# Kernel tuning notes

Hardware: AMD Instinct MI355X
Metric: run time of the kernel (lower is better)

Reference implementation:

```python
import jax, jax.numpy as jnp
import numpy as np

WS = 8            # window size (square)
N = WS * WS       # tokens per window = 64
DIM = 192
HEADS = 6
HDIM = DIM // HEADS
SCALE = HDIM ** -0.5


def _rel_pos_index(ws=WS):
    coords = np.stack(np.meshgrid(np.arange(ws), np.arange(ws), indexing='ij'))  # [2,ws,ws]
    cf = coords.reshape(2, -1)                       # [2, N]
    rc = (cf[:, :, None] - cf[:, None, :]).transpose(1, 2, 0).astype(np.int64)  # [N,N,2]
    rc[:, :, 0] += ws - 1
    rc[:, :, 1] += ws - 1
    rc[:, :, 0] *= 2 * ws - 1
    return jnp.asarray(rc.sum(-1))                   # [N, N]

REL_IDX = _rel_pos_index()


def _linear(x, w, b=None):
    y = jnp.einsum('...i,oi->...o', x, w)
    return y if b is None else y + b


def _diff_attn(q_t, k_t, v_t, q_r, k_r, v_r, bias, lam):
    # q,k,v: [B, H, N, d]; bias: [H, N, N]; lam scalar
    at = jax.nn.softmax(jnp.einsum('bhqd,bhkd->bhqk', q_t * SCALE, k_t) + bias, axis=-1)
    ar = jax.nn.softmax(jnp.einsum('bhqd,bhkd->bhqk', q_r * SCALE, k_r) + bias, axis=-1)
    dt = at - lam * ar
    dr = ar - lam * at
    ot = jnp.einsum('bhqk,bhkd->bhqd', dt, v_t)
    orf = jnp.einsum('bhqk,bhkd->bhqd', dr, v_r)
    return ot, orf


def _heads(x, B):
    # [B, N, C] -> [B, H, N, d]
    return x.reshape(B, N, HEADS, HDIM).transpose(0, 2, 1, 3)


def _unheads(x, B):
    return x.transpose(0, 2, 1, 3).reshape(B, N, DIM)


def setup_inputs() -> dict:
    key = jax.random.key(0)
    ks = jax.random.split(key, 16)
    nW = 1024
    p = lambda k, shp: (jax.random.normal(k, shp, jnp.float32) * 0.02)
    return {
        'x_windows': jax.random.normal(ks[0], (nW, N, DIM), jnp.float32),
        'y_windows': jax.random.normal(ks[1], (nW, N, DIM), jnp.float32),
        'sa_qkv_w': p(ks[2], (3 * DIM, DIM)), 'sa_qkv_b': jnp.zeros((3 * DIM,), jnp.float32),
        'sa_ct_w': p(ks[3], (DIM, DIM)), 'sa_cr_w': p(ks[4], (DIM, DIM)),
        'ca_q_w': p(ks[5], (DIM, DIM)), 'ca_q_b': jnp.zeros((DIM,), jnp.float32),
        'ca_kv_w': p(ks[6], (2 * DIM, DIM)), 'ca_kv_b': jnp.zeros((2 * DIM,), jnp.float32),
        'ca_ct_w': p(ks[7], (DIM, DIM)), 'ca_cr_w': p(ks[8], (DIM, DIM)),
        'rpb_table': p(ks[9], ((2 * WS - 1) * (2 * WS - 1), HEADS)),
        'proj_sa_w': p(ks[10], (DIM, DIM)), 'proj_sa_b': jnp.zeros((DIM,), jnp.float32),
        'proj_ca_w': p(ks[11], (DIM, DIM)), 'proj_ca_b': jnp.zeros((DIM,), jnp.float32),
        'lambda_sa': jnp.float32(0.1), 'lambda_ca': jnp.float32(0.1),
        'sa_enh': jnp.float32(0.1), 'ca_enh': jnp.float32(0.1),
    }


def reference(x_windows, y_windows, sa_qkv_w, sa_qkv_b, sa_ct_w, sa_cr_w,
              ca_q_w, ca_q_b, ca_kv_w, ca_kv_b, ca_ct_w, ca_cr_w,
              rpb_table, proj_sa_w, proj_sa_b, proj_ca_w, proj_ca_b,
              lambda_sa, lambda_ca, sa_enh, ca_enh):
    B = x_windows.shape[0]
    bias = rpb_table[REL_IDX.reshape(-1)].reshape(N, N, HEADS).transpose(2, 0, 1)  # [H,N,N]

    # ---- Self-attention branch (batch-dim concat) ----
    t_enh = x_windows + sa_enh * _linear(y_windows, sa_cr_w)
    r_enh = y_windows + sa_enh * _linear(x_windows, sa_ct_w)
    qkv_t = _linear(t_enh, sa_qkv_w, sa_qkv_b).reshape(B, N, 3, HEADS, HDIM).transpose(2, 0, 3, 1, 4)
    qkv_r = _linear(r_enh, sa_qkv_w, sa_qkv_b).reshape(B, N, 3, HEADS, HDIM).transpose(2, 0, 3, 1, 4)
    lam_sa = jnp.clip(jax.nn.sigmoid(lambda_sa), 0.01, 0.99)
    ot, orf = _diff_attn(qkv_t[0], qkv_t[1], qkv_t[2], qkv_r[0], qkv_r[1], qkv_r[2], bias, lam_sa)
    sa_t = _linear(_unheads(ot, B), proj_sa_w, proj_sa_b)
    sa_r = _linear(_unheads(orf, B), proj_sa_w, proj_sa_b)
    sa_out = jnp.concatenate([sa_t, sa_r], axis=0)  # [2B, N, C]

    # ---- Cross-attention branch (seq-dim concat) ----
    t_enh = x_windows + ca_enh * _linear(y_windows, ca_cr_w)
    r_enh = y_windows + ca_enh * _linear(x_windows, ca_ct_w)
    q_t = _heads(_linear(t_enh, ca_q_w, ca_q_b), B)
    q_r = _heads(_linear(r_enh, ca_q_w, ca_q_b), B)
    xcat = jnp.concatenate([t_enh, r_enh], axis=1)  # [B, 2N, C]
    kv = _linear(xcat, ca_kv_w, ca_kv_b).reshape(B, 2 * N, 2, HEADS, HDIM).transpose(2, 0, 3, 1, 4)
    k, v = kv[0], kv[1]
    k_t, k_r = k[:, :, :N], k[:, :, N:]
    v_t, v_r = v[:, :, :N], v[:, :, N:]
    lam_ca = jnp.clip(jax.nn.sigmoid(lambda_ca), 0.01, 0.99)
    ot, orf = _diff_attn(q_t, k_t, v_t, q_r, k_r, v_r, bias, lam_ca)
    ca_t = _linear(_unheads(ot, B), proj_ca_w, proj_ca_b)
    ca_r = _linear(_unheads(orf, B), proj_ca_w, proj_ca_b)
    ca_out = jnp.concatenate([ca_t, ca_r], axis=1)  # [B, 2N, C]

    # pack into a single array: [4B, N, C]
    return jnp.concatenate([sa_out, ca_out.reshape(2 * B, N, DIM)], axis=0)
```

## Files before the change

### kernel.cpp

```cpp
#include <hip/hip_runtime.h>

#define KD 192
#define H6 6

typedef __attribute__((ext_vector_type(8))) short bf16x8;
typedef __attribute__((ext_vector_type(4))) float f32x4;

__device__ __forceinline__ unsigned short f2bf(float f) {
  unsigned u = __float_as_uint(f);
  u += 0x7FFFu + ((u >> 16) & 1u);
  return (unsigned short)(u >> 16);
}

__global__ void bias_k(const float* __restrict__ tab, float* __restrict__ biasw) {
  int t = blockIdx.x * 256 + threadIdx.x;
  if (t >= H6 * 64 * 64) return;
  int h = t >> 12, rem = t & 4095, i = rem >> 6, j = rem & 63;
  int idx = ((i >> 3) - (j >> 3) + 7) * 15 + ((i & 7) - (j & 7) + 7);
  biasw[t] = tab[idx * H6 + h];
}

__global__ void convert_k(
    const float* __restrict__ sa_qkv_w, const float* __restrict__ sa_ct_w,
    const float* __restrict__ sa_cr_w, const float* __restrict__ ca_q_w,
    const float* __restrict__ ca_kv_w, const float* __restrict__ ca_ct_w,
    const float* __restrict__ ca_cr_w, const float* __restrict__ proj_sa_w,
    const float* __restrict__ proj_ca_w,
    const float* __restrict__ ca_q_b, const float* __restrict__ ca_kv_b,
    unsigned short* __restrict__ wqkv, unsigned short* __restrict__ wct_sa,
    unsigned short* __restrict__ wcr_sa, unsigned short* __restrict__ wca,
    unsigned short* __restrict__ wct_ca, unsigned short* __restrict__ wcr_ca,
    unsigned short* __restrict__ wpsa, unsigned short* __restrict__ wpca,
    float* __restrict__ bca)
{
  int t = blockIdx.x * 256 + threadIdx.x;
  if (t < 110592) {
    int i = t << 2;
    const float* s; unsigned short* d;
    if (i < 110592)      { s = sa_qkv_w + i;            d = wqkv + i; }
    else if (i < 147456) { s = sa_ct_w + (i - 110592);  d = wct_sa + (i - 110592); }
    else if (i < 184320) { s = sa_cr_w + (i - 147456);  d = wcr_sa + (i - 147456); }
    else if (i < 221184) { s = ca_q_w + (i - 184320);   d = wca + (i - 184320); }
    else if (i < 294912) { s = ca_kv_w + (i - 221184);  d = wca + 36864 + (i - 221184); }
    else if (i < 331776) { s = ca_ct_w + (i - 294912);  d = wct_ca + (i - 294912); }
    else if (i < 368640) { s = ca_cr_w + (i - 331776);  d = wcr_ca + (i - 331776); }
    else if (i < 405504) { s = proj_sa_w + (i - 368640); d = wpsa + (i - 368640); }
    else                 { s = proj_ca_w + (i - 405504); d = wpca + (i - 405504); }
    float4 v = *(const float4*)s;
    ushort4 p;
    p.x = f2bf(v.x); p.y = f2bf(v.y); p.z = f2bf(v.z); p.w = f2bf(v.w);
    *(ushort4*)d = p;
  } else if (t < 110592 + 144) {
    int i = (t - 110592) << 2;
    const float* s = (i < 192) ? (ca_q_b + i) : (ca_kv_b + (i - 192));
    *(float4*)(bca + i) = *(const float4*)s;
  }
}

__global__ __launch_bounds__(256) void enh_k(
    const float* __restrict__ x, const float* __restrict__ y,
    const unsigned short* __restrict__ wcr_sa, const unsigned short* __restrict__ wct_sa,
    const unsigned short* __restrict__ wcr_ca, const unsigned short* __restrict__ wct_ca,
    const float* __restrict__ sap, const float* __restrict__ cap,
    unsigned short* __restrict__ e0, unsigned short* __restrict__ e1,
    unsigned short* __restrict__ e2, unsigned short* __restrict__ e3)
{
  __shared__ short Xl[64][200], Yl[64][200], Wl[64][200];
  const int tid = threadIdx.x;
  const int nblk = blockIdx.x, mblk = blockIdx.y;
  const int row = tid >> 2, cb = (tid & 3) * 48;
  {
    const float* xp = x + ((long)mblk * 64 + row) * KD + cb;
    const float* yp = y + ((long)mblk * 64 + row) * KD + cb;
#pragma unroll
    for (int j = 0; j < 12; ++j) {
      float4 vx = *(const float4*)(xp + 4 * j);
      float4 vy = *(const float4*)(yp + 4 * j);
      ushort4 px, py;
      px.x = f2bf(vx.x); px.y = f2bf(vx.y); px.z = f2bf(vx.z); px.w = f2bf(vx.w);
      py.x = f2bf(vy.x); py.y = f2bf(vy.y); py.z = f2bf(vy.z); py.w = f2bf(vy.w);
      *(ushort4*)&Xl[row][cb + 4 * j] = px;
      *(ushort4*)&Yl[row][cb + 4 * j] = py;
    }
  }
  const unsigned short* Ws[4] = {wcr_sa, wct_sa, wcr_ca, wct_ca};
  unsigned short* Es[4] = {e0, e1, e2, e3};
  const float s_sa = *sap, s_ca = *cap;

  const int lane = tid & 63, wv = tid >> 6;
  const int qn = lane & 15, g = lane >> 4;
  const int mloc = 16 * wv + 4 * g;
  const f32x4 zero = {0.f, 0.f, 0.f, 0.f};

  for (int it = 0; it < 4; ++it) {
    {
      const unsigned short* Wp = Ws[it] + ((long)nblk * 64 + row) * KD + cb;
#pragma unroll
      for (int j = 0; j < 6; ++j)
        *(float4*)&Wl[row][cb + 8 * j] = *(const float4*)(Wp + 8 * j);
    }
    __syncthreads();
    short (*Aloc)[200] = (it & 1) ? Xl : Yl;
    f32x4 acc[4];
#pragma unroll
    for (int nt = 0; nt < 4; ++nt) acc[nt] = zero;
#pragma unroll
    for (int ks = 0; ks < 6; ++ks) {
      bf16x8 a = *(const bf16x8*)&Aloc[16 * wv + qn][32 * ks + 8 * g];
#pragma unroll
      for (int nt = 0; nt < 4; ++nt) {
        bf16x8 bfr = *(const bf16x8*)&Wl[16 * nt + qn][32 * ks + 8 * g];
        acc[nt] = __builtin_amdgcn_mfma_f32_16x16x32_bf16(a, bfr, acc[nt], 0, 0, 0);
      }
    }
    const float* resid = (it & 1) ? y : x;
    const float sc = (it < 2) ? s_sa : s_ca;
    unsigned short* dst = Es[it];
#pragma unroll
    for (int nt = 0; nt < 4; ++nt) {
      const int c = nblk * 64 + 16 * nt + qn;
#pragma unroll
      for (int r = 0; r < 4; ++r) {
        const long m = (long)mblk * 64 + mloc + r;
        dst[m * KD + c] = f2bf(resid[m * KD + c] + sc * acc[nt][r]);
      }
    }
    __syncthreads();
  }
}

struct QkvArgs {
  const unsigned short* A[4];
  const unsigned short* W[4];
  const float* bias[4];
  unsigned short* dq[4];
  unsigned short* dk[4];
  unsigned short* dv[4];
};

__global__ __launch_bounds__(256) void qkv_k(QkvArgs args, float SC)
{
  __shared__ short Al[64][200], Wl[64][200];
  const int tid = threadIdx.x;
  const int nblk = blockIdx.x, mblk = blockIdx.y, z = blockIdx.z;
  const int row = tid >> 2, cb = (tid & 3) * 48;
  {
    const unsigned short* A = args.A[z] + ((long)mblk * 64 + row) * KD + cb;
#pragma unroll
    for (int j = 0; j < 6; ++j)
      *(float4*)&Al[row][cb + 8 * j] = *(const float4*)(A + 8 * j);
    const unsigned short* Wp = args.W[z] + ((long)nblk * 64 + row) * KD + cb;
#pragma unroll
    for (int j = 0; j < 6; ++j)
      *(float4*)&Wl[row][cb + 8 * j] = *(const float4*)(Wp + 8 * j);
  }
  __syncthreads();

  const int lane = tid & 63, wv = tid >> 6;
  const int qn = lane & 15, g = lane >> 4;
  const f32x4 zero = {0.f, 0.f, 0.f, 0.f};
  f32x4 acc[4];
#pragma unroll
  for (int nt = 0; nt < 4; ++nt) acc[nt] = zero;
#pragma unroll
  for (int ks = 0; ks < 6; ++ks) {
    bf16x8 a = *(const bf16x8*)&Al[16 * wv + qn][32 * ks + 8 * g];
#pragma unroll
    for (int nt = 0; nt < 4; ++nt) {
      bf16x8 bfr = *(const bf16x8*)&Wl[16 * nt + qn][32 * ks + 8 * g];
      acc[nt] = __builtin_amdgcn_mfma_f32_16x16x32_bf16(a, bfr, acc[nt], 0, 0, 0);
    }
  }
  const int mloc = 16 * wv + 4 * g;
#pragma unroll
  for (int nt = 0; nt < 4; ++nt) {
    const int cg = nblk * 64 + 16 * nt + qn;
    const int idx = (cg >= 384) ? 2 : ((cg >= 192) ? 1 : 0);
    const int cc = cg - idx * KD;
    const int h = cc >> 5, d = cc & 31;
    const float bv = args.bias[z][cg];
    const float sca = (idx == 0) ? SC : 1.f;
    const long bwh = (long)mblk * H6 + h;
    if (idx < 2) {
      unsigned short* dst = idx ? args.dk[z] : args.dq[z];
#pragma unroll
      for (int r = 0; r < 4; ++r)
        dst[(bwh * 64 + (mloc + r)) * 32 + d] = f2bf((acc[nt][r] + bv) * sca);
    } else {
      ushort4 p;
      p.x = f2bf(acc[nt][0] + bv);
      p.y = f2bf(acc[nt][1] + bv);
      p.z = f2bf(acc[nt][2] + bv);
      p.w = f2bf(acc[nt][3] + bv);
      *(ushort4*)&args.dv[z][(bwh * 32 + d) * 64 + mloc] = p;
    }
  }
}

struct ProjArgs {
  const unsigned short* A[4];
  const unsigned short* W[4];
  const float* bias[4];
  float* o[4];
  long wstride[4];
};

__global__ __launch_bounds__(256) void proj_k(ProjArgs args)
{
  __shared__ short Al[64][200], Wl[64][200];
  const int tid = threadIdx.x;
  const int nblk = blockIdx.x, mblk = blockIdx.y, z = blockIdx.z;
  const int row = tid >> 2, cb = (tid & 3) * 48;
  {
    const unsigned short* A = args.A[z] + ((long)mblk * 64 + row) * KD + cb;
#pragma unroll
    for (int j = 0; j < 6; ++j)
      *(float4*)&Al[row][cb + 8 * j] = *(const float4*)(A + 8 * j);
    const unsigned short* Wp = args.W[z] + ((long)nblk * 64 + row) * KD + cb;
#pragma unroll
    for (int j = 0; j < 6; ++j)
      *(float4*)&Wl[row][cb + 8 * j] = *(const float4*)(Wp + 8 * j);
  }
  __syncthreads();

  const int lane = tid & 63, wv = tid >> 6;
  const int qn = lane & 15, g = lane >> 4;
  const f32x4 zero = {0.f, 0.f, 0.f, 0.f};
  f32x4 acc[4];
#pragma unroll
  for (int nt = 0; nt < 4; ++nt) acc[nt] = zero;
#pragma unroll
  for (int ks = 0; ks < 6; ++ks) {
    bf16x8 a = *(const bf16x8*)&Al[16 * wv + qn][32 * ks + 8 * g];
#pragma unroll
    for (int nt = 0; nt < 4; ++nt) {
      bf16x8 bfr = *(const bf16x8*)&Wl[16 * nt + qn][32 * ks + 8 * g];
      acc[nt] = __builtin_amdgcn_mfma_f32_16x16x32_bf16(a, bfr, acc[nt], 0, 0, 0);
    }
  }
  const int mloc = 16 * wv + 4 * g;
  float* fo = args.o[z] + (long)mblk * args.wstride[z];
#pragma unroll
  for (int nt = 0; nt < 4; ++nt) {
    const int c = nblk * 64 + 16 * nt + qn;
    const float bv = args.bias[z][c];
#pragma unroll
    for (int r = 0; r < 4; ++r)
      fo[(long)(mloc + r) * KD + c] = acc[nt][r] + bv;
  }
}

__device__ __forceinline__ void softmax_rows2(f32x4 (&S)[4][2]) {
#pragma unroll
  for (int nt = 0; nt < 2; ++nt) {
    float mx = -3.0e38f;
#pragma unroll
    for (int mt = 0; mt < 4; ++mt)
#pragma unroll
      for (int r = 0; r < 4; ++r) mx = fmaxf(mx, S[mt][nt][r]);
    mx = fmaxf(mx, __shfl_xor(mx, 16));
    mx = fmaxf(mx, __shfl_xor(mx, 32));
    float sm = 0.f;
#pragma unroll
    for (int mt = 0; mt < 4; ++mt)
#pragma unroll
      for (int r = 0; r < 4; ++r) {
        float p = __expf(S[mt][nt][r] - mx);
        S[mt][nt][r] = p;
        sm += p;
      }
    sm += __shfl_xor(sm, 16);
    sm += __shfl_xor(sm, 32);
    const float inv = 1.f / sm;
#pragma unroll
    for (int mt = 0; mt < 4; ++mt)
#pragma unroll
      for (int r = 0; r < 4; ++r) S[mt][nt][r] *= inv;
  }
}

__device__ __forceinline__ void diff_attn32(
    const unsigned short* __restrict__ qb, const unsigned short* __restrict__ kb,
    const unsigned short* __restrict__ vTb, long pstride,
    const float* __restrict__ bh, float lam,
    unsigned short* __restrict__ o_t, unsigned short* __restrict__ o_r,
    long base, int b, int h, int qoff, int qn, int g,
    short (*Pl)[32][72])
{
  f32x4 st[4][2], sr[4][2];
#pragma unroll
  for (int mt = 0; mt < 4; ++mt)
#pragma unroll
    for (int nt = 0; nt < 2; ++nt) {
      f32x4 bv = *(const f32x4*)&bh[(qoff + 16 * nt + qn) * 64 + 16 * mt + 4 * g];
      st[mt][nt] = bv;
      sr[mt][nt] = bv;
    }
  {
    bf16x8 ka[4], qv[2];
#pragma unroll
    for (int mt = 0; mt < 4; ++mt)
      ka[mt] = *(const bf16x8*)&kb[base + (16 * mt + qn) * 32 + 8 * g];
#pragma unroll
    for (int nt = 0; nt < 2; ++nt)
      qv[nt] = *(const bf16x8*)&qb[base + (qoff + 16 * nt + qn) * 32 + 8 * g];
#pragma unroll
    for (int mt = 0; mt < 4; ++mt)
#pragma unroll
      for (int nt = 0; nt < 2; ++nt)
        st[mt][nt] = __builtin_amdgcn_mfma_f32_16x16x32_bf16(ka[mt], qv[nt], st[mt][nt], 0, 0, 0);
#pragma unroll
    for (int mt = 0; mt < 4; ++mt)
      ka[mt] = *(const bf16x8*)&kb[pstride + base + (16 * mt + qn) * 32 + 8 * g];
#pragma unroll
    for (int nt = 0; nt < 2; ++nt)
      qv[nt] = *(const bf16x8*)&qb[pstride + base + (qoff + 16 * nt + qn) * 32 + 8 * g];
#pragma unroll
    for (int mt = 0; mt < 4; ++mt)
#pragma unroll
      for (int nt = 0; nt < 2; ++nt)
        sr[mt][nt] = __builtin_amdgcn_mfma_f32_16x16x32_bf16(ka[mt], qv[nt], sr[mt][nt], 0, 0, 0);
  }
  softmax_rows2(st);
  softmax_rows2(sr);
#pragma unroll
  for (int mt = 0; mt < 4; ++mt)
#pragma unroll
    for (int nt = 0; nt < 2; ++nt) {
      ushort4 pt, pr;
#pragma unroll
      for (int r = 0; r < 4; ++r) {
        float a = st[mt][nt][r], rr = sr[mt][nt][r];
        ((unsigned short*)&pt)[r] = f2bf(a - lam * rr);
        ((unsigned short*)&pr)[r] = f2bf(rr - lam * a);
      }
      *(ushort4*)&Pl[0][16 * nt + qn][16 * mt + 4 * g] = pt;
      *(ushort4*)&Pl[1][16 * nt + qn][16 * mt + 4 * g] = pr;
    }
  const f32x4 zero = {0.f, 0.f, 0.f, 0.f};
#pragma unroll
  for (int p = 0; p < 2; ++p) {
    const unsigned short* vv = p ? (vTb + pstride) : vTb;
    unsigned short* outp = p ? o_r : o_t;
    f32x4 oa[2][2];
#pragma unroll
    for (int i = 0; i < 2; ++i)
#pragma unroll
      for (int nt = 0; nt < 2; ++nt) oa[i][nt] = zero;
#pragma unroll
    for (int ks = 0; ks < 2; ++ks) {
      bf16x8 va0 = *(const bf16x8*)&vv[base + (0 + qn) * 64 + 32 * ks + 8 * g];
      bf16x8 va1 = *(const bf16x8*)&vv[base + (16 + qn) * 64 + 32 * ks + 8 * g];
#pragma unroll
      for (int nt = 0; nt < 2; ++nt) {
        bf16x8 pb = *(const bf16x8*)&Pl[p][16 * nt + qn][32 * ks + 8 * g];
        oa[0][nt] = __builtin_amdgcn_mfma_f32_16x16x32_bf16(va0, pb, oa[0][nt], 0, 0, 0);
        oa[1][nt] = __builtin_amdgcn_mfma_f32_16x16x32_bf16(va1, pb, oa[1][nt], 0, 0, 0);
      }
    }
#pragma unroll
    for (int d16 = 0; d16 < 2; ++d16)
#pragma unroll
      for (int nt = 0; nt < 2; ++nt) {
        const int q = qoff + 16 * nt + qn;
        ushort4 pk;
        pk.x = f2bf(oa[d16][nt][0]); pk.y = f2bf(oa[d16][nt][1]);
        pk.z = f2bf(oa[d16][nt][2]); pk.w = f2bf(oa[d16][nt][3]);
        *(ushort4*)&outp[((long)b * 64 + q) * KD + h * 32 + 16 * d16 + 4 * g] = pk;
      }
  }
}

__global__ __launch_bounds__(256) void attn_k(
    const unsigned short* __restrict__ saq, const unsigned short* __restrict__ sak,
    const unsigned short* __restrict__ savT,
    const unsigned short* __restrict__ caq, const unsigned short* __restrict__ cak,
    const unsigned short* __restrict__ cavT,
    const float* __restrict__ biasw, const float* __restrict__ lsp,
    const float* __restrict__ lcp,
    unsigned short* __restrict__ o0, unsigned short* __restrict__ o1,
    unsigned short* __restrict__ o2, unsigned short* __restrict__ o3,
    long pstride)
{
  __shared__ short Pl[4][2][32][72];
  const int wv = threadIdx.x >> 6, lane = threadIdx.x & 63;
  const int qn = lane & 15, g = lane >> 4;
  const int qoff = (wv & 1) * 32;
  const int wh = blockIdx.x * 2 + (wv >> 1);
  const int b = wh / H6, h = wh - b * H6;
  const float* bh = biasw + (long)h * 4096;
  const long base = (long)wh * 2048;
  float ls = 1.f / (1.f + __expf(-*lsp));
  ls = fminf(fmaxf(ls, 0.01f), 0.99f);
  float lc = 1.f / (1.f + __expf(-*lcp));
  lc = fminf(fmaxf(lc, 0.01f), 0.99f);
  diff_attn32(saq, sak, savT, pstride, bh, ls, o0, o1, base, b, h, qoff, qn, g, Pl[wv]);
  diff_attn32(caq, cak, cavT, pstride, bh, lc, o2, o3, base, b, h, qoff, qn, g, Pl[wv]);
}

extern "C" void kernel_launch(void* const* d_in, const int* in_sizes, int n_in,
                              void* d_out, int out_size, void* d_ws, size_t ws_size,
                              hipStream_t stream)
{
  const float* x         = (const float*)d_in[0];
  const float* y         = (const float*)d_in[1];
  const float* sa_qkv_w  = (const float*)d_in[2];
  const float* sa_qkv_b  = (const float*)d_in[3];
  const float* sa_ct_w   = (const float*)d_in[4];
  const float* sa_cr_w   = (const float*)d_in[5];
  const float* ca_q_w    = (const float*)d_in[6];
  const float* ca_q_b    = (const float*)d_in[7];
  const float* ca_kv_w   = (const float*)d_in[8];
  const float* ca_kv_b   = (const float*)d_in[9];
  const float* ca_ct_w   = (const float*)d_in[10];
  const float* ca_cr_w   = (const float*)d_in[11];
  const float* rpb       = (const float*)d_in[12];
  const float* proj_sa_w = (const float*)d_in[13];
  const float* proj_sa_b = (const float*)d_in[14];
  const float* proj_ca_w = (const float*)d_in[15];
  const float* proj_ca_b = (const float*)d_in[16];
  const float* lam_sa_p  = (const float*)d_in[17];
  const float* lam_ca_p  = (const float*)d_in[18];
  const float* sa_enh_p  = (const float*)d_in[19];
  const float* ca_enh_p  = (const float*)d_in[20];
  float* out = (float*)d_out;

  const int M = in_sizes[0] / KD;
  const int B = M / 64;
  const long pstride = (long)B * H6 * 2048;

  char* ws = (char*)d_ws;
  float* biasw = (float*)ws;
  float* bca = (float*)(ws + 98304);
  unsigned short* wqkv   = (unsigned short*)(ws + 100864);
  unsigned short* wca    = (unsigned short*)(ws + 322048);
  unsigned short* wct_sa = (unsigned short*)(ws + 543232);
  unsigned short* wcr_sa = (unsigned short*)(ws + 616960);
  unsigned short* wct_ca = (unsigned short*)(ws + 690688);
  unsigned short* wcr_ca = (unsigned short*)(ws + 764416);
  unsigned short* wpsa   = (unsigned short*)(ws + 838144);
  unsigned short* wpca   = (unsigned short*)(ws + 911872);
  long off = 1048576;
  unsigned short* enh0 = (unsigned short*)(ws + off); off += (long)M * KD * 2;
  unsigned short* enh1 = (unsigned short*)(ws + off); off += (long)M * KD * 2;
  unsigned short* enh2 = (unsigned short*)(ws + off); off += (long)M * KD * 2;
  unsigned short* enh3 = (unsigned short*)(ws + off); off += (long)M * KD * 2;
  unsigned short* caq  = (unsigned short*)(ws + off); off += pstride * 4;
  unsigned short* cak  = (unsigned short*)(ws + off); off += pstride * 4;
  unsigned short* cavT = (unsigned short*)(ws + off); off += pstride * 4;
  unsigned short* saq  = (unsigned short*)d_out;
  unsigned short* sak  = saq + 2 * pstride;
  unsigned short* savT = sak + 2 * pstride;

  const float SC = 0.17677669529663687f;

  convert_k<<<dim3(433), dim3(256), 0, stream>>>(
      sa_qkv_w, sa_ct_w, sa_cr_w, ca_q_w, ca_kv_w, ca_ct_w, ca_cr_w,
      proj_sa_w, proj_ca_w, ca_q_b, ca_kv_b,
      wqkv, wct_sa, wcr_sa, wca, wct_ca, wcr_ca, wpsa, wpca, bca);
  bias_k<<<dim3(96), dim3(256), 0, stream>>>(rpb, biasw);

  enh_k<<<dim3(3, B), dim3(256), 0, stream>>>(x, y, wcr_sa, wct_sa, wcr_ca, wct_ca,
                                              sa_enh_p, ca_enh_p, enh0, enh1, enh2, enh3);

  QkvArgs qa;
  qa.A[0] = enh0; qa.A[1] = enh1; qa.A[2] = enh2; qa.A[3] = enh3;
  qa.W[0] = wqkv; qa.W[1] = wqkv; qa.W[2] = wca; qa.W[3] = wca;
  qa.bias[0] = sa_qkv_b; qa.bias[1] = sa_qkv_b; qa.bias[2] = bca; qa.bias[3] = bca;
  qa.dq[0] = saq;  qa.dq[1] = saq + pstride;  qa.dq[2] = caq;  qa.dq[3] = caq + pstride;
  qa.dk[0] = sak;  qa.dk[1] = sak + pstride;  qa.dk[2] = cak;  qa.dk[3] = cak + pstride;
  qa.dv[0] = savT; qa.dv[1] = savT + pstride; qa.dv[2] = cavT; qa.dv[3] = cavT + pstride;
  qkv_k<<<dim3(9, B, 4), dim3(256), 0, stream>>>(qa, SC);

  attn_k<<<dim3(B * H6 / 2), dim3(256), 0, stream>>>(saq, sak, savT, caq, cak, cavT,
                                                     biasw, lam_sa_p, lam_ca_p,
                                                     enh0, enh1, enh2, enh3, pstride);

  ProjArgs pa;
  pa.A[0] = enh0; pa.A[1] = enh1; pa.A[2] = enh2; pa.A[3] = enh3;
  pa.W[0] = wpsa; pa.W[1] = wpsa; pa.W[2] = wpca; pa.W[3] = wpca;
  pa.bias[0] = proj_sa_b; pa.bias[1] = proj_sa_b; pa.bias[2] = proj_ca_b; pa.bias[3] = proj_ca_b;
  pa.o[0] = out;                       pa.wstride[0] = 12288;
  pa.o[1] = out + (long)B * 12288;     pa.wstride[1] = 12288;
  pa.o[2] = out + (long)2 * B * 12288; pa.wstride[2] = 24576;
  pa.o[3] = out + (long)2 * B * 12288 + 12288; pa.wstride[3] = 24576;
  proj_k<<<dim3(3, B, 4), dim3(256), 0, stream>>>(pa);
}
```

Before: 779.4 us.

## Fuse enhancement GEMM into QKV projection kernel and loop N-tiles per block

Merges the cross-modal enhancement GEMM into the QKV kernel. Each block now computes its 64-row enhanced tile in shared memory and then loops over all nine QKV weight tiles, so the enhanced activations no longer round-trip through global memory and one launch is removed. The output projection kernel likewise loops over its three column tiles per block instead of spreading them across the grid, which reuses the A tile. The cost is much less grid parallelism (B×4 blocks instead of 9×B×4), more LDS per block and longer serial per-block work with a sync after every tile.

```diff
diff --git a/kernel.cpp b/kernel.cpp
--- a/kernel.cpp
+++ b/kernel.cpp
@@ -57,143 +57,118 @@
   }
 }
 
-__global__ __launch_bounds__(256) void enh_k(
-    const float* __restrict__ x, const float* __restrict__ y,
-    const unsigned short* __restrict__ wcr_sa, const unsigned short* __restrict__ wct_sa,
-    const unsigned short* __restrict__ wcr_ca, const unsigned short* __restrict__ wct_ca,
-    const float* __restrict__ sap, const float* __restrict__ cap,
-    unsigned short* __restrict__ e0, unsigned short* __restrict__ e1,
-    unsigned short* __restrict__ e2, unsigned short* __restrict__ e3)
-{
-  __shared__ short Xl[64][200], Yl[64][200], Wl[64][200];
-  const int tid = threadIdx.x;
-  const int nblk = blockIdx.x, mblk = blockIdx.y;
-  const int row = tid >> 2, cb = (tid & 3) * 48;
-  {
-    const float* xp = x + ((long)mblk * 64 + row) * KD + cb;
-    const float* yp = y + ((long)mblk * 64 + row) * KD + cb;
-#pragma unroll
-    for (int j = 0; j < 12; ++j) {
-      float4 vx = *(const float4*)(xp + 4 * j);
-      float4 vy = *(const float4*)(yp + 4 * j);
-      ushort4 px, py;
-      px.x = f2bf(vx.x); px.y = f2bf(vx.y); px.z = f2bf(vx.z); px.w = f2bf(vx.w);
-      py.x = f2bf(vy.x); py.y = f2bf(vy.y); py.z = f2bf(vy.z); py.w = f2bf(vy.w);
-      *(ushort4*)&Xl[row][cb + 4 * j] = px;
-      *(ushort4*)&Yl[row][cb + 4 * j] = py;
-    }
-  }
-  const unsigned short* Ws[4] = {wcr_sa, wct_sa, wcr_ca, wct_ca};
-  unsigned short* Es[4] = {e0, e1, e2, e3};
-  const float s_sa = *sap, s_ca = *cap;
-
-  const int lane = tid & 63, wv = tid >> 6;
-  const int qn = lane & 15, g = lane >> 4;
-  const int mloc = 16 * wv + 4 * g;
-  const f32x4 zero = {0.f, 0.f, 0.f, 0.f};
-
-  for (int it = 0; it < 4; ++it) {
-    {
-      const unsigned short* Wp = Ws[it] + ((long)nblk * 64 + row) * KD + cb;
-#pragma unroll
-      for (int j = 0; j < 6; ++j)
-        *(float4*)&Wl[row][cb + 8 * j] = *(const float4*)(Wp + 8 * j);
-    }
-    __syncthreads();
-    short (*Aloc)[200] = (it & 1) ? Xl : Yl;
-    f32x4 acc[4];
-#pragma unroll
-    for (int nt = 0; nt < 4; ++nt) acc[nt] = zero;
-#pragma unroll
-    for (int ks = 0; ks < 6; ++ks) {
-      bf16x8 a = *(const bf16x8*)&Aloc[16 * wv + qn][32 * ks + 8 * g];
-#pragma unroll
-      for (int nt = 0; nt < 4; ++nt) {
-        bf16x8 bfr = *(const bf16x8*)&Wl[16 * nt + qn][32 * ks + 8 * g];
-        acc[nt] = __builtin_amdgcn_mfma_f32_16x16x32_bf16(a, bfr, acc[nt], 0, 0, 0);
-      }
-    }
-    const float* resid = (it & 1) ? y : x;
-    const float sc = (it < 2) ? s_sa : s_ca;
-    unsigned short* dst = Es[it];
-#pragma unroll
-    for (int nt = 0; nt < 4; ++nt) {
-      const int c = nblk * 64 + 16 * nt + qn;
-#pragma unroll
-      for (int r = 0; r < 4; ++r) {
-        const long m = (long)mblk * 64 + mloc + r;
-        dst[m * KD + c] = f2bf(resid[m * KD + c] + sc * acc[nt][r]);
-      }
-    }
-    __syncthreads();
-  }
-}
-
-struct QkvArgs {
-  const unsigned short* A[4];
-  const unsigned short* W[4];
+struct FQArgs {
+  const unsigned short* Wc[4];
+  const unsigned short* Wq[4];
   const float* bias[4];
   unsigned short* dq[4];
   unsigned short* dk[4];
   unsigned short* dv[4];
 };
 
-__global__ __launch_bounds__(256) void qkv_k(QkvArgs args, float SC)
-{
-  __shared__ short Al[64][200], Wl[64][200];
+__global__ __launch_bounds__(256) void fqkv_k(
+    const float* __restrict__ x, const float* __restrict__ y,
+    const float* __restrict__ sap, const float* __restrict__ cap,
+    FQArgs args, float SC)
+{
+  __shared__ short Al[64][200], Wl[64][200], El[64][200];
   const int tid = threadIdx.x;
-  const int nblk = blockIdx.x, mblk = blockIdx.y, z = blockIdx.z;
+  const int mblk = blockIdx.x, z = blockIdx.y;
   const int row = tid >> 2, cb = (tid & 3) * 48;
+  const float* A    = (z & 1) ? x : y;
+  const float* resd = (z & 1) ? y : x;
+  const float sc = (z < 2) ? *sap : *cap;
+
   {
-    const unsigned short* A = args.A[z] + ((long)mblk * 64 + row) * KD + cb;
-#pragma unroll
-    for (int j = 0; j < 6; ++j)
-      *(float4*)&Al[row][cb + 8 * j] = *(const float4*)(A + 8 * j);
-    const unsigned short* Wp = args.W[z] + ((long)nblk * 64 + row) * KD + cb;
-#pragma unroll
-    for (int j = 0; j < 6; ++j)
-      *(float4*)&Wl[row][cb + 8 * j] = *(const float4*)(Wp + 8 * j);
-  }
-  __syncthreads();
-
+    const float* ap = A + ((long)mblk * 64 + row) * KD + cb;
+#pragma unroll
+    for (int j = 0; j < 12; ++j) {
+      float4 v = *(const float4*)(ap + 4 * j);
+      ushort4 p;
+      p.x = f2bf(v.x); p.y = f2bf(v.y); p.z = f2bf(v.z); p.w = f2bf(v.w);
+      *(ushort4*)&Al[row][cb + 4 * j] = p;
+    }
+  }
   const int lane = tid & 63, wv = tid >> 6;
   const int qn = lane & 15, g = lane >> 4;
+  const int mloc = 16 * wv + 4 * g;
   const f32x4 zero = {0.f, 0.f, 0.f, 0.f};
-  f32x4 acc[4];
-#pragma unroll
-  for (int nt = 0; nt < 4; ++nt) acc[nt] = zero;
-#pragma unroll
-  for (int ks = 0; ks < 6; ++ks) {
-    bf16x8 a = *(const bf16x8*)&Al[16 * wv + qn][32 * ks + 8 * g];
+
+  for (int ct = 0; ct < 3; ++ct) {
+    {
+      const unsigned short* Wp = args.Wc[z] + ((long)ct * 64 + row) * KD + cb;
+#pragma unroll
+      for (int j = 0; j < 6; ++j)
+        *(float4*)&Wl[row][cb + 8 * j] = *(const float4*)(Wp + 8 * j);
+    }
+    __syncthreads();
+    f32x4 acc[4];
+#pragma unroll
+    for (int nt = 0; nt < 4; ++nt) acc[nt] = zero;
+#pragma unroll
+    for (int ks = 0; ks < 6; ++ks) {
+      bf16x8 a = *(const bf16x8*)&Al[16 * wv + qn][32 * ks + 8 * g];
+#pragma unroll
+      for (int nt = 0; nt < 4; ++nt) {
+        bf16x8 bfr = *(const bf16x8*)&Wl[16 * nt + qn][32 * ks + 8 * g];
+        acc[nt] = __builtin_amdgcn_mfma_f32_16x16x32_bf16(a, bfr, acc[nt], 0, 0, 0);
+      }
+    }
 #pragma unroll
     for (int nt = 0; nt < 4; ++nt) {
-      bf16x8 bfr = *(const bf16x8*)&Wl[16 * nt + qn][32 * ks + 8 * g];
-      acc[nt] = __builtin_amdgcn_mfma_f32_16x16x32_bf16(a, bfr, acc[nt], 0, 0, 0);
-    }
-  }
-  const int mloc = 16 * wv + 4 * g;
-#pragma unroll
-  for (int nt = 0; nt < 4; ++nt) {
-    const int cg = nblk * 64 + 16 * nt + qn;
-    const int idx = (cg >= 384) ? 2 : ((cg >= 192) ? 1 : 0);
-    const int cc = cg - idx * KD;
-    const int h = cc >> 5, d = cc & 31;
-    const float bv = args.bias[z][cg];
-    const float sca = (idx == 0) ? SC : 1.f;
-    const long bwh = (long)mblk * H6 + h;
-    if (idx < 2) {
-      unsigned short* dst = idx ? args.dk[z] : args.dq[z];
+      const int c = ct * 64 + 16 * nt + qn;
 #pragma unroll
       for (int r = 0; r < 4; ++r)
-        dst[(bwh * 64 + (mloc + r)) * 32 + d] = f2bf((acc[nt][r] + bv) * sca);
-    } else {
-      ushort4 p;
-      p.x = f2bf(acc[nt][0] + bv);
-      p.y = f2bf(acc[nt][1] + bv);
-      p.z = f2bf(acc[nt][2] + bv);
-      p.w = f2bf(acc[nt][3] + bv);
-      *(ushort4*)&args.dv[z][(bwh * 32 + d) * 64 + mloc] = p;
-    }
+        El[mloc + r][c] =
+            f2bf(resd[((long)mblk * 64 + mloc + r) * KD + c] + sc * acc[nt][r]);
+    }
+    __syncthreads();
+  }
+
+  for (int wt = 0; wt < 9; ++wt) {
+    {
+      const unsigned short* Wp = args.Wq[z] + ((long)wt * 64 + row) * KD + cb;
+#pragma unroll
+      for (int j = 0; j < 6; ++j)
+        *(float4*)&Wl[row][cb + 8 * j] = *(const float4*)(Wp + 8 * j);
+    }
+    __syncthreads();
+    f32x4 acc[4];
+#pragma unroll
+    for (int nt = 0; nt < 4; ++nt) acc[nt] = zero;
+#pragma unroll
+    for (int ks = 0; ks < 6; ++ks) {
+      bf16x8 a = *(const bf16x8*)&El[16 * wv + qn][32 * ks + 8 * g];
+#pragma unroll
+      for (int nt = 0; nt < 4; ++nt) {
+        bf16x8 bfr = *(const bf16x8*)&Wl[16 * nt + qn][32 * ks + 8 * g];
+        acc[nt] = __builtin_amdgcn_mfma_f32_16x16x32_bf16(a, bfr, acc[nt], 0, 0, 0);
+      }
+    }
+#pragma unroll
+    for (int nt = 0; nt < 4; ++nt) {
+      const int cg = wt * 64 + 16 * nt + qn;
+      const int idx = (cg >= 384) ? 2 : ((cg >= 192) ? 1 : 0);
+      const int cc = cg - idx * KD;
+      const int h = cc >> 5, d = cc & 31;
+      const float bv = args.bias[z][cg];
+      const float sca = (idx == 0) ? SC : 1.f;
+      const long bwh = (long)mblk * H6 + h;
+      if (idx < 2) {
+        unsigned short* dst = idx ? args.dk[z] : args.dq[z];
+#pragma unroll
+        for (int r = 0; r < 4; ++r)
+          dst[(bwh * 64 + (mloc + r)) * 32 + d] = f2bf((acc[nt][r] + bv) * sca);
+      } else {
+        ushort4 p;
+        p.x = f2bf(acc[nt][0] + bv);
+        p.y = f2bf(acc[nt][1] + bv);
+        p.z = f2bf(acc[nt][2] + bv);
+        p.w = f2bf(acc[nt][3] + bv);
+        *(ushort4*)&args.dv[z][(bwh * 32 + d) * 64 + mloc] = p;
+      }
+    }
+    __syncthreads();
   }
 }
 
@@ -209,44 +184,49 @@
 {
   __shared__ short Al[64][200], Wl[64][200];
   const int tid = threadIdx.x;
-  const int nblk = blockIdx.x, mblk = blockIdx.y, z = blockIdx.z;
+  const int mblk = blockIdx.x, z = blockIdx.y;
   const int row = tid >> 2, cb = (tid & 3) * 48;
   {
     const unsigned short* A = args.A[z] + ((long)mblk * 64 + row) * KD + cb;
 #pragma unroll
     for (int j = 0; j < 6; ++j)
       *(float4*)&Al[row][cb + 8 * j] = *(const float4*)(A + 8 * j);
-    const unsigned short* Wp = args.W[z] + ((long)nblk * 64 + row) * KD + cb;
-#pragma unroll
-    for (int j = 0; j < 6; ++j)
-      *(float4*)&Wl[row][cb + 8 * j] = *(const float4*)(Wp + 8 * j);
-  }
-  __syncthreads();
-
+  }
   const int lane = tid & 63, wv = tid >> 6;
   const int qn = lane & 15, g = lane >> 4;
+  const int mloc = 16 * wv + 4 * g;
   const f32x4 zero = {0.f, 0.f, 0.f, 0.f};
-  f32x4 acc[4];
-#pragma unroll
-  for (int nt = 0; nt < 4; ++nt) acc[nt] = zero;
-#pragma unroll
-  for (int ks = 0; ks < 6; ++ks) {
-    bf16x8 a = *(const bf16x8*)&Al[16 * wv + qn][32 * ks + 8 * g];
+  float* fo = args.o[z] + (long)mblk * args.wstride[z];
+
+  for (int ct = 0; ct < 3; ++ct) {
+    {
+      const unsigned short* Wp = args.W[z] + ((long)ct * 64 + row) * KD + cb;
+#pragma unroll
+      for (int j = 0; j < 6; ++j)
+        *(float4*)&Wl[row][cb + 8 * j] = *(const float4*)(Wp + 8 * j);
+    }
+    __syncthreads();
+    f32x4 acc[4];
+#pragma unroll
+    for (int nt = 0; nt < 4; ++nt) acc[nt] = zero;
+#pragma unroll
+    for (int ks = 0; ks < 6; ++ks) {
+      bf16x8 a = *(const bf16x8*)&Al[16 * wv + qn][32 * ks + 8 * g];
+#pragma unroll
+      for (int nt = 0; nt < 4; ++nt) {
+        bf16x8 bfr = *(const bf16x8*)&Wl[16 * nt + qn][32 * ks + 8 * g];
+        acc[nt] = __builtin_amdgcn_mfma_f32_16x16x32_bf16(a, bfr, acc[nt], 0, 0, 0);
+      }
+    }
 #pragma unroll
     for (int nt = 0; nt < 4; ++nt) {
-      bf16x8 bfr = *(const bf16x8*)&Wl[16 * nt + qn][32 * ks + 8 * g];
-      acc[nt] = __builtin_amdgcn_mfma_f32_16x16x32_bf16(a, bfr, acc[nt], 0, 0, 0);
-    }
-  }
-  const int mloc = 16 * wv + 4 * g;
-  float* fo = args.o[z] + (long)mblk * args.wstride[z];
-#pragma unroll
-  for (int nt = 0; nt < 4; ++nt) {
-    const int c = nblk * 64 + 16 * nt + qn;
-    const float bv = args.bias[z][c];
-#pragma unroll
-    for (int r = 0; r < 4; ++r)
-      fo[(long)(mloc + r) * KD + c] = acc[nt][r] + bv;
+      const int c = ct * 64 + 16 * nt + qn;
+      const float bv = args.bias[z][c];
+#pragma unroll
+      for (int r = 0; r < 4; ++r)
+        fo[(long)(mloc + r) * KD + c] = acc[nt][r] + bv;
+    }
+    __syncthreads();
   }
 }
 
@@ -441,10 +421,10 @@
   unsigned short* wpsa   = (unsigned short*)(ws + 838144);
   unsigned short* wpca   = (unsigned short*)(ws + 911872);
   long off = 1048576;
-  unsigned short* enh0 = (unsigned short*)(ws + off); off += (long)M * KD * 2;
-  unsigned short* enh1 = (unsigned short*)(ws + off); off += (long)M * KD * 2;
-  unsigned short* enh2 = (unsigned short*)(ws + off); off += (long)M * KD * 2;
-  unsigned short* enh3 = (unsigned short*)(ws + off); off += (long)M * KD * 2;
+  unsigned short* ob0 = (unsigned short*)(ws + off); off += (long)M * KD * 2;
+  unsigned short* ob1 = (unsigned short*)(ws + off); off += (long)M * KD * 2;
+  unsigned short* ob2 = (unsigned short*)(ws + off); off += (long)M * KD * 2;
+  unsigned short* ob3 = (unsigned short*)(ws + off); off += (long)M * KD * 2;
   unsigned short* caq  = (unsigned short*)(ws + off); off += pstride * 4;
   unsigned short* cak  = (unsigned short*)(ws + off); off += pstride * 4;
   unsigned short* cavT = (unsigned short*)(ws + off); off += pstride * 4;
@@ -460,29 +440,26 @@
       wqkv, wct_sa, wcr_sa, wca, wct_ca, wcr_ca, wpsa, wpca, bca);
   bias_k<<<dim3(96), dim3(256), 0, stream>>>(rpb, biasw);
 
-  enh_k<<<dim3(3, B), dim3(256), 0, stream>>>(x, y, wcr_sa, wct_sa, wcr_ca, wct_ca,
-                                              sa_enh_p, ca_enh_p, enh0, enh1, enh2, enh3);
-
-  QkvArgs qa;
-  qa.A[0] = enh0; qa.A[1] = enh1; qa.A[2] = enh2; qa.A[3] = enh3;
-  qa.W[0] = wqkv; qa.W[1] = wqkv; qa.W[2] = wca; qa.W[3] = wca;
-  qa.bias[0] = sa_qkv_b; qa.bias[1] = sa_qkv_b; qa.bias[2] = bca; qa.bias[3] = bca;
-  qa.dq[0] = saq;  qa.dq[1] = saq + pstride;  qa.dq[2] = caq;  qa.dq[3] = caq + pstride;
-  qa.dk[0] = sak;  qa.dk[1] = sak + pstride;  qa.dk[2] = cak;  qa.dk[3] = cak + pstride;
-  qa.dv[0] = savT; qa.dv[1] = savT + pstride; qa.dv[2] = cavT; qa.dv[3] = cavT + pstride;
-  qkv_k<<<dim3(9, B, 4), dim3(256), 0, stream>>>(qa, SC);
+  FQArgs fa;
+  fa.Wc[0] = wcr_sa; fa.Wc[1] = wct_sa; fa.Wc[2] = wcr_ca; fa.Wc[3] = wct_ca;
+  fa.Wq[0] = wqkv;   fa.Wq[1] = wqkv;   fa.Wq[2] = wca;    fa.Wq[3] = wca;
+  fa.bias[0] = sa_qkv_b; fa.bias[1] = sa_qkv_b; fa.bias[2] = bca; fa.bias[3] = bca;
+  fa.dq[0] = saq;  fa.dq[1] = saq + pstride;  fa.dq[2] = caq;  fa.dq[3] = caq + pstride;
+  fa.dk[0] = sak;  fa.dk[1] = sak + pstride;  fa.dk[2] = cak;  fa.dk[3] = cak + pstride;
+  fa.dv[0] = savT; fa.dv[1] = savT + pstride; fa.dv[2] = cavT; fa.dv[3] = cavT + pstride;
+  fqkv_k<<<dim3(B, 4), dim3(256), 0, stream>>>(x, y, sa_enh_p, ca_enh_p, fa, SC);
 
   attn_k<<<dim3(B * H6 / 2), dim3(256), 0, stream>>>(saq, sak, savT, caq, cak, cavT,
                                                      biasw, lam_sa_p, lam_ca_p,
-                                                     enh0, enh1, enh2, enh3, pstride);
+                                                     ob0, ob1, ob2, ob3, pstride);
 
   ProjArgs pa;
-  pa.A[0] = enh0; pa.A[1] = enh1; pa.A[2] = enh2; pa.A[3] = enh3;
+  pa.A[0] = ob0; pa.A[1] = ob1; pa.A[2] = ob2; pa.A[3] = ob3;
   pa.W[0] = wpsa; pa.W[1] = wpsa; pa.W[2] = wpca; pa.W[3] = wpca;
   pa.bias[0] = proj_sa_b; pa.bias[1] = proj_sa_b; pa.bias[2] = proj_ca_b; pa.bias[3] = proj_ca_b;
   pa.o[0] = out;                       pa.wstride[0] = 12288;
   pa.o[1] = out + (long)B * 12288;     pa.wstride[1] = 12288;
   pa.o[2] = out + (long)2 * B * 12288; pa.wstride[2] = 24576;
   pa.o[3] = out + (long)2 * B * 12288 + 12288; pa.wstride[3] = 24576;
-  proj_k<<<dim3(3, B, 4), dim3(256), 0, stream>>>(pa);
-}
+  proj_k<<<dim3(B, 4), dim3(256), 0, stream>>>(pa);
+}
```

Measured after the change: 665.6 us. 1.17x faster.
